# Kernel optimization log

Measured on AMD Instinct MI355X. Metric: run time of the kernel, lower is better.

The kernel has to match this reference:

```python
import jax, jax.numpy as jnp
import numpy as np

DIM_HID = 65536
NKERS = 500  # fixed by nn.Linear(dim_hid, 500) in the original module


def setup_inputs() -> dict:
    key = jax.random.key(0)
    k1, k2, k3, k4, k5 = jax.random.split(key, 5)
    inp = jax.random.normal(k1, (DIM_HID,), dtype=jnp.float32)
    weight = jax.random.normal(k2, (NKERS, DIM_HID), dtype=jnp.float32) * (1.0 / np.sqrt(DIM_HID))
    bias = jax.random.normal(k3, (NKERS,), dtype=jnp.float32)
    # variable-width kernels, each kwidths[i] in [1, NKERS]
    kwidths = jax.random.randint(k4, (NKERS,), 1, NKERS + 1, dtype=jnp.int32)
    kernels = jax.random.normal(k5, (NKERS, NKERS), dtype=jnp.float32)
    return {"input": inp, "weight": weight, "bias": bias, "kernels": kernels, "kwidths": kwidths}


def reference(input, weight, bias, kernels, kwidths):
    # y = self.coefs(input): [NKERS]
    y = weight @ input + bias
    # The torch loop  z[:kwidths[i]] += y[i] * kernels[i]  is exactly a
    # weighted sum of zero-padded kernel rows: mask row i beyond kwidths[i].
    col = jnp.arange(NKERS, dtype=kwidths.dtype)
    mask = col[None, :] < kwidths[:, None]            # [NKERS, NKERS] bool
    padded = jnp.where(mask, kernels, 0.0)            # zero-padded kernel bank
    z = y @ padded                                    # [NKERS]
    return z
```

## Files before the change

kernel.cpp:

```cpp
#include <hip/hip_runtime.h>

#define DIM_HID 65536
#define NKERS   500

__global__ __launch_bounds__(1024) void gemv_kernel(
    const float* __restrict__ W,
    const float* __restrict__ x,
    const float* __restrict__ b,
    float* __restrict__ y)
{
    const int row = blockIdx.x;
    const float4* __restrict__ Wrow =
        reinterpret_cast<const float4*>(W + (size_t)row * DIM_HID);
    const float4* __restrict__ xv = reinterpret_cast<const float4*>(x);

    const int t = threadIdx.x;
    float sum = 0.0f;
#pragma unroll
    for (int k = 0; k < 16; ++k) {
        const int idx = t + k * 1024;
        float4 w = Wrow[idx];
        float4 v = xv[idx];
        sum = fmaf(w.x, v.x, sum);
        sum = fmaf(w.y, v.y, sum);
        sum = fmaf(w.z, v.z, sum);
        sum = fmaf(w.w, v.w, sum);
    }

#pragma unroll
    for (int off = 32; off > 0; off >>= 1)
        sum += __shfl_down(sum, off, 64);

    __shared__ float wsum[16];
    const int wave = t >> 6;
    const int lane = t & 63;
    if (lane == 0) wsum[wave] = sum;
    __syncthreads();

    if (t == 0) {
        float s = 0.0f;
#pragma unroll
        for (int w = 0; w < 16; ++w) s += wsum[w];
        y[row] = s + b[row];
    }
}

__global__ __launch_bounds__(256) void expand_kernel(
    const float* __restrict__ y,
    const float* __restrict__ kernels,
    const int* __restrict__ kw,
    float* __restrict__ z)
{
    const int j = blockIdx.x;
    const int t = threadIdx.x;

    float acc = 0.0f;
#pragma unroll
    for (int k = 0; k < 2; ++k) {
        const int i = t + k * 256;
        if (i < NKERS) {
            const float yi = y[i];
            const int   w  = kw[i];
            const float kv = kernels[i * NKERS + j];
            if (j < w) acc = fmaf(yi, kv, acc);
        }
    }

#pragma unroll
    for (int off = 32; off > 0; off >>= 1)
        acc += __shfl_down(acc, off, 64);

    __shared__ float wsum[4];
    const int wave = t >> 6;
    const int lane = t & 63;
    if (lane == 0) wsum[wave] = acc;
    __syncthreads();

    if (t == 0)
        z[j] = (wsum[0] + wsum[1]) + (wsum[2] + wsum[3]);
}

extern "C" void kernel_launch(void* const* d_in, const int* in_sizes, int n_in,
                              void* d_out, int out_size, void* d_ws, size_t ws_size,
                              hipStream_t stream)
{
    const float* input   = (const float*)d_in[0];
    const float* weight  = (const float*)d_in[1];
    const float* bias    = (const float*)d_in[2];
    const float* kernels = (const float*)d_in[3];
    const int*   kwidths = (const int*)d_in[4];
    float* z = (float*)d_out;
    float* y = (float*)d_ws;

    gemv_kernel<<<NKERS, 1024, 0, stream>>>(weight, input, bias, y);
    expand_kernel<<<NKERS, 256, 0, stream>>>(y, kernels, kwidths, z);
}
```

Before: 33.62 us.

## Split GEMV rows into four partial blocks and reduce partials in expand kernel

The GEMV now launches 2000 blocks of 256 threads, each covering one quarter of a weight row and writing a partial sum to the workspace. The expand kernel adds the four partials and the bias when it reads each coefficient. Weight loads become nontemporal and the inner loop unroll drops to 4. The aim is finer-grained parallelism and better load balance and occupancy on the memory-bound 131 MB weight stream. The cost is more blocks, extra partial-sum traffic, and redundant partial reduction in every expand block.

```diff
diff --git a/kernel.cpp b/kernel.cpp
--- a/kernel.cpp
+++ b/kernel.cpp
@@ -2,64 +2,70 @@
 
 #define DIM_HID 65536
 #define NKERS   500
+#define NQ      4
+#define QCHUNK  (DIM_HID / NQ)
 
-__global__ __launch_bounds__(1024) void gemv_kernel(
+typedef float f4 __attribute__((ext_vector_type(4)));
+
+__global__ __launch_bounds__(256) void gemv_part_kernel(
     const float* __restrict__ W,
     const float* __restrict__ x,
-    const float* __restrict__ b,
-    float* __restrict__ y)
+    float* __restrict__ ws)
 {
-    const int row = blockIdx.x;
-    const float4* __restrict__ Wrow =
-        reinterpret_cast<const float4*>(W + (size_t)row * DIM_HID);
-    const float4* __restrict__ xv = reinterpret_cast<const float4*>(x);
+    const int bid = blockIdx.x;
+    const int row = bid >> 2;
+    const int q   = bid & 3;
+    const int t   = threadIdx.x;
 
-    const int t = threadIdx.x;
-    float sum = 0.0f;
-#pragma unroll
+    const f4* __restrict__ Wq =
+        reinterpret_cast<const f4*>(W + (size_t)row * DIM_HID + q * QCHUNK);
+    const f4* __restrict__ xq =
+        reinterpret_cast<const f4*>(x + q * QCHUNK);
+
+    float s = 0.0f;
+#pragma unroll 4
     for (int k = 0; k < 16; ++k) {
-        const int idx = t + k * 1024;
-        float4 w = Wrow[idx];
-        float4 v = xv[idx];
-        sum = fmaf(w.x, v.x, sum);
-        sum = fmaf(w.y, v.y, sum);
-        sum = fmaf(w.z, v.z, sum);
-        sum = fmaf(w.w, v.w, sum);
+        const int idx = t + k * 256;
+        f4 w = __builtin_nontemporal_load(&Wq[idx]);
+        f4 v = xq[idx];
+        s = fmaf(w.x, v.x, s);
+        s = fmaf(w.y, v.y, s);
+        s = fmaf(w.z, v.z, s);
+        s = fmaf(w.w, v.w, s);
     }
 
 #pragma unroll
     for (int off = 32; off > 0; off >>= 1)
-        sum += __shfl_down(sum, off, 64);
+        s += __shfl_down(s, off, 64);
 
-    __shared__ float wsum[16];
+    __shared__ float wsum[4];
     const int wave = t >> 6;
     const int lane = t & 63;
-    if (lane == 0) wsum[wave] = sum;
+    if (lane == 0) wsum[wave] = s;
     __syncthreads();
 
-    if (t == 0) {
-        float s = 0.0f;
-#pragma unroll
-        for (int w = 0; w < 16; ++w) s += wsum[w];
-        y[row] = s + b[row];
-    }
+    if (t == 0)
+        ws[bid] = (wsum[0] + wsum[1]) + (wsum[2] + wsum[3]);
 }
 
 __global__ __launch_bounds__(256) void expand_kernel(
-    const float* __restrict__ y,
+    const float* __restrict__ ws,
+    const float* __restrict__ bias,
     const float* __restrict__ kernels,
     const int* __restrict__ kw,
     float* __restrict__ z)
 {
     const int j = blockIdx.x;
     const int t = threadIdx.x;
+    const f4* __restrict__ wsv = reinterpret_cast<const f4*>(ws);
 
     float acc = 0.0f;
 #pragma unroll
     for (int k = 0; k < 2; ++k) {
         const int i = t + k * 256;
         if (i < NKERS) {
-            const float yi = y[i];
+            f4 p = wsv[i];
+            const float yi = ((p.x + p.y) + (p.z + p.w)) + bias[i];
             const int   w  = kw[i];
             const float kv = kernels[i * NKERS + j];
             if (j < w) acc = fmaf(yi, kv, acc);
@@ -89,9 +95,9 @@
     const float* bias    = (const float*)d_in[2];
     const float* kernels = (const float*)d_in[3];
     const int*   kwidths = (const int*)d_in[4];
-    float* z = (float*)d_out;
-    float* y = (float*)d_ws;
+    float* z  = (float*)d_out;
+    float* ws = (float*)d_ws;
 
-    gemv_kernel<<<NKERS, 1024, 0, stream>>>(weight, input, bias, y);
-    expand_kernel<<<NKERS, 256, 0, stream>>>(y, kernels, kwidths, z);
+    gemv_part_kernel<<<NKERS * NQ, 256, 0, stream>>>(weight, input, ws);
+    expand_kernel<<<NKERS, 256, 0, stream>>>(ws, bias, kernels, kwidths, z);
 }
```

New measurement: 29.76 us. -11.5%, faster.
